# Optimization experiments

Measured on AMD Instinct MI355X. Metric: run time of the kernel, lower is better.

## Reference

```python
import jax, jax.numpy as jnp
import numpy as np

EPS = 1e-8  # matches PairwiseCosine eps clamp


def setup_inputs() -> dict:
    key = jax.random.key(0)
    k1, k2, k3 = jax.random.split(key, 3)
    B, N, M, D = 8, 2048, 2048, 256
    desc_src = jax.random.normal(k1, (B, N, D), dtype=jnp.float32)
    desc_dst = jax.random.normal(k2, (B, M, D), dtype=jnp.float32)
    points_dst = jax.random.uniform(k3, (B, M, 2), dtype=jnp.float32)
    return {"desc_src": desc_src, "desc_dst": desc_dst, "points_dst": points_dst}


def reference(desc_src, desc_dst, points_dst):
    # Pairwise cosine similarity: [B, N, M]
    xx = jnp.linalg.norm(desc_src, axis=-1, keepdims=True)          # [B, N, 1]
    yy = jnp.linalg.norm(desc_dst, axis=-1, keepdims=True)          # [B, M, 1]
    xy = jnp.einsum('bnd,bmd->bnm', desc_src, desc_dst)             # [B, N, M]
    sim = xy / jnp.maximum(xx * jnp.swapaxes(yy, 1, 2), EPS)
    # Best match per source descriptor
    confidence = jnp.max(sim, axis=2)                               # [B, N]
    idx = jnp.argmax(sim, axis=2)                                   # [B, N]
    # Gather matched destination points: [B, N, 2]
    matched = jnp.take_along_axis(points_dst, idx[:, :, None], axis=1)
    return (matched, confidence)
```

## Files before the change

kernel.cpp:

```cpp
#include <hip/hip_runtime.h>
#include <stdint.h>

constexpr int Bq = 8, Nq = 2048, Mq = 2048, Dq = 256;
constexpr int TILE = 128;
constexpr int KC = 32;
constexpr int NCH = Dq / KC;
constexpr int LDS_S = 40;

typedef float f32x4 __attribute__((ext_vector_type(4)));
typedef _Float16 f16x8 __attribute__((ext_vector_type(8)));
typedef _Float16 f16x4 __attribute__((ext_vector_type(4)));
typedef __fp16 fp16x2 __attribute__((ext_vector_type(2)));

__device__ __forceinline__ uint32_t f2sortable(float f) {
  uint32_t u = __float_as_uint(f);
  return (u & 0x80000000u) ? ~u : (u | 0x80000000u);
}
__device__ __forceinline__ float sortable2f(uint32_t s) {
  uint32_t u = (s & 0x80000000u) ? (s ^ 0x80000000u) : ~s;
  return __uint_as_float(u);
}

__device__ __forceinline__ void load16(float* d, const float* __restrict__ p) {
  *(float4*)&d[0]  = *(const float4*)(p + 0);
  *(float4*)&d[4]  = *(const float4*)(p + 4);
  *(float4*)&d[8]  = *(const float4*)(p + 8);
  *(float4*)&d[12] = *(const float4*)(p + 12);
}

__device__ __forceinline__ void split8(const float* x, f16x8* hi, f16x8* lo,
                                       float& sq) {
  union { f16x8 v; fp16x2 p[4]; } H, L;
#pragma unroll
  for (int j = 0; j < 4; ++j) {
    float x0 = x[2 * j], x1 = x[2 * j + 1];
    sq = fmaf(x0, x0, sq);
    sq = fmaf(x1, x1, sq);
    float h0 = __uint_as_float(__float_as_uint(x0) & 0xFFFFE000u);
    float h1 = __uint_as_float(__float_as_uint(x1) & 0xFFFFE000u);
    H.p[j] = __builtin_amdgcn_cvt_pkrtz(h0, h1);
    L.p[j] = __builtin_amdgcn_cvt_pkrtz(x0 - h0, x1 - h1);
  }
  *hi = H.v;
  *lo = L.v;
}


__global__ __launch_bounds__(256)
void prep_kernel(const float* __restrict__ src, const float* __restrict__ dst,
                 _Float16* __restrict__ Ah, _Float16* __restrict__ Al,
                 _Float16* __restrict__ Bh, _Float16* __restrict__ Bl,
                 float* __restrict__ invnx, float* __restrict__ invny) {
  const int lane = threadIdx.x & 63;
  const int wv = threadIdx.x >> 6;
  const int r = blockIdx.x * 4 + wv;

  const float* x;
  _Float16 *h, *l;
  float* inv;
  if (blockIdx.y == 0) { x = src; h = Ah; l = Al; inv = invnx; }
  else                 { x = dst; h = Bh; l = Bl; inv = invny; }

  float4 v = *(const float4*)(x + (size_t)r * Dq + lane * 4);
  float sq = 0.f;
  union { f16x4 v; fp16x2 p[2]; } H, L;
  float e[4] = {v.x, v.y, v.z, v.w};
#pragma unroll
  for (int j = 0; j < 2; ++j) {
    float x0 = e[2 * j], x1 = e[2 * j + 1];
    sq = fmaf(x0, x0, sq);
    sq = fmaf(x1, x1, sq);
    float h0 = __uint_as_float(__float_as_uint(x0) & 0xFFFFE000u);
    float h1 = __uint_as_float(__float_as_uint(x1) & 0xFFFFE000u);
    H.p[j] = __builtin_amdgcn_cvt_pkrtz(h0, h1);
    L.p[j] = __builtin_amdgcn_cvt_pkrtz(x0 - h0, x1 - h1);
  }
#pragma unroll
  for (int m = 1; m <= 32; m <<= 1) sq += __shfl_xor(sq, m);

  const int b = r >> 11, row = r & 2047;
  const int c = lane >> 3, ko = (lane & 7) * 4;
  size_t idx = ((size_t)(b * NCH + c) * 2048 + row) * KC + ko;
  *(f16x4*)&h[idx] = H.v;
  *(f16x4*)&l[idx] = L.v;
  if (lane == 0) inv[r] = 1.0f / sqrtf(sq);
}

__device__ __forceinline__ void stage(const _Float16* g, _Float16* l, int lane) {
  const char* gc = (const char*)g + lane * 16;
  char* lc = (char*)l;
#pragma unroll
  for (int i = 0; i < 8; ++i)
    __builtin_amdgcn_global_load_lds(
        (const __attribute__((address_space(1))) void*)(gc + i * 1024),
        (__attribute__((address_space(3))) void*)(lc + i * 1024),
        16, 0, 0);
}


__global__ __launch_bounds__(256, 2)
void simmax_mfma(const _Float16* __restrict__ Ah, const _Float16* __restrict__ Al,
                 const _Float16* __restrict__ Bh, const _Float16* __restrict__ Bl,
                 const float* __restrict__ invnx, const float* __restrict__ invny,
                 unsigned long long* __restrict__ best) {
  __shared__ __align__(16) _Float16 lds[2][4][TILE][KC];

  const int orig = blockIdx.x;
  const int logical = (orig & 7) * 256 + (orig >> 3);
  const int b = logical >> 8;
  const int nt = (logical >> 4) & 15;
  const int mt = logical & 15;

  const int tid = threadIdx.x;
  const int lane = tid & 63;
  const int wave = tid >> 6;
  const int wy = wave >> 1, wx = wave & 1;
  const int ln15 = lane & 15, lq = lane >> 4;

  const _Float16* garr = (wave == 0) ? Ah : (wave == 1) ? Al
                        : (wave == 2) ? Bh : Bl;
  const int grow = ((wave < 2) ? nt : mt) * TILE;
  const _Float16* g0 = garr + ((size_t)(b * NCH) * 2048 + grow) * KC;
  constexpr size_t CSTR = (size_t)2048 * KC;

  f32x4 acc[4][4];
#pragma unroll
  for (int i = 0; i < 4; ++i)
#pragma unroll
    for (int j = 0; j < 4; ++j) acc[i][j] = (f32x4){0.f, 0.f, 0.f, 0.f};

  stage(g0, &lds[0][wave][0][0], lane);
  __syncthreads();

#pragma unroll
  for (int c = 0; c < NCH; ++c) {
    const int cb = c & 1;
    if (c + 1 < NCH)
      stage(g0 + (size_t)(c + 1) * CSTR, &lds[cb ^ 1][wave][0][0], lane);

    f16x8 bhf[4], blf[4];
#pragma unroll
    for (int ct = 0; ct < 4; ++ct) {
      const int rb = wx * 64 + ct * 16 + ln15;
      bhf[ct] = *(const f16x8*)&lds[cb][2][rb][lq * 8];
      blf[ct] = *(const f16x8*)&lds[cb][3][rb][lq * 8];
    }
#pragma unroll
    for (int rt = 0; rt < 4; ++rt) {
      const int ra = wy * 64 + rt * 16 + ln15;
      f16x8 ahf = *(const f16x8*)&lds[cb][0][ra][lq * 8];
      f16x8 alf = *(const f16x8*)&lds[cb][1][ra][lq * 8];
#pragma unroll
      for (int ct = 0; ct < 4; ++ct) {
        acc[rt][ct] = __builtin_amdgcn_mfma_f32_16x16x32_f16(ahf, bhf[ct], acc[rt][ct], 0, 0, 0);
        acc[rt][ct] = __builtin_amdgcn_mfma_f32_16x16x32_f16(ahf, blf[ct], acc[rt][ct], 0, 0, 0);
        acc[rt][ct] = __builtin_amdgcn_mfma_f32_16x16x32_f16(alf, bhf[ct], acc[rt][ct], 0, 0, 0);
      }
    }
    if (c + 1 < NCH) __syncthreads();
  }

  float invy[4];
#pragma unroll
  for (int ct = 0; ct < 4; ++ct)
    invy[ct] = invny[(size_t)b * Mq + mt * TILE + wx * 64 + ct * 16 + ln15];

#pragma unroll
  for (int rt = 0; rt < 4; ++rt) {
#pragma unroll
    for (int reg = 0; reg < 4; ++reg) {
      float bq = -1e30f;
      int bc = 0x7FFFFFFF;
#pragma unroll
      for (int ct = 0; ct < 4; ++ct) {
        float q = acc[rt][ct][reg] * invy[ct];
        int cg = mt * TILE + wx * 64 + ct * 16 + ln15;
        if (q > bq || (q == bq && cg < bc)) { bq = q; bc = cg; }
      }
#pragma unroll
      for (int m = 1; m <= 8; m <<= 1) {
        float q2 = __shfl_xor(bq, m);
        int c2 = __shfl_xor(bc, m);
        if (q2 > bq || (q2 == bq && c2 < bc)) { bq = q2; bc = c2; }
      }
      if (ln15 == 0) {
        int rloc = wy * 64 + rt * 16 + lq * 4 + reg;
        float conf = bq * invnx[(size_t)b * Nq + nt * TILE + rloc];
        unsigned long long p =
            ((unsigned long long)(f2sortable(conf) ^ 0x80000000u) << 32) |
            (uint32_t)(~(uint32_t)bc);
        atomicMax((long long*)&best[(size_t)b * Nq + nt * TILE + rloc],
                  (long long)p);
      }
    }
  }
}

__global__ __launch_bounds__(256, 3)
void simmax_kernel(const float* __restrict__ src, const float* __restrict__ dst,
                   unsigned long long* __restrict__ best) {
  __shared__ _Float16 Ah[TILE][LDS_S], Al[TILE][LDS_S];
  __shared__ _Float16 Bh[TILE][LDS_S], Bl[TILE][LDS_S];
  __shared__ float invnx_s[TILE], invny_s[TILE];

  const int b = blockIdx.z, nt = blockIdx.y, mt = blockIdx.x;
  const int tid = threadIdx.x;
  const int lane = tid & 63;
  const int wave = tid >> 6;
  const int wy = wave >> 1, wx = wave & 1;
  const int ln15 = lane & 15, lq = lane >> 4;

  const int sr = tid >> 1;
  const int sk = (tid & 1) * 16;
  const float* Ag = src + ((size_t)(b * Nq + nt * TILE + sr)) * Dq + sk;
  const float* Bg = dst + ((size_t)(b * Mq + mt * TILE + sr)) * Dq + sk;

  f32x4 acc[4][4];
#pragma unroll
  for (int i = 0; i < 4; ++i)
#pragma unroll
    for (int j = 0; j < 4; ++j) acc[i][j] = (f32x4){0.f, 0.f, 0.f, 0.f};
  float sqa = 0.f, sqb = 0.f;

  float av[16], bv[16];
  load16(av, Ag);
  load16(bv, Bg);

  for (int c = 0; c < NCH; ++c) {
    f16x8 ah2[2], al2[2], bh2[2], bl2[2];
    split8(&av[0], &ah2[0], &al2[0], sqa);
    split8(&av[8], &ah2[1], &al2[1], sqa);
    split8(&bv[0], &bh2[0], &bl2[0], sqb);
    split8(&bv[8], &bh2[1], &bl2[1], sqb);
    __syncthreads();
    *(f16x8*)&Ah[sr][sk]     = ah2[0];
    *(f16x8*)&Ah[sr][sk + 8] = ah2[1];
    *(f16x8*)&Al[sr][sk]     = al2[0];
    *(f16x8*)&Al[sr][sk + 8] = al2[1];
    *(f16x8*)&Bh[sr][sk]     = bh2[0];
    *(f16x8*)&Bh[sr][sk + 8] = bh2[1];
    *(f16x8*)&Bl[sr][sk]     = bl2[0];
    *(f16x8*)&Bl[sr][sk + 8] = bl2[1];
    __syncthreads();

    if (c + 1 < NCH) {
      load16(av, Ag + (c + 1) * KC);
      load16(bv, Bg + (c + 1) * KC);
    }

    f16x8 bhf[4], blf[4];
#pragma unroll
    for (int ct = 0; ct < 4; ++ct) {
      int rowb = wx * 64 + ct * 16 + ln15;
      bhf[ct] = *(const f16x8*)&Bh[rowb][lq * 8];
      blf[ct] = *(const f16x8*)&Bl[rowb][lq * 8];
    }
#pragma unroll
    for (int rt = 0; rt < 4; ++rt) {
      int rowa = wy * 64 + rt * 16 + ln15;
      f16x8 ahf = *(const f16x8*)&Ah[rowa][lq * 8];
      f16x8 alf = *(const f16x8*)&Al[rowa][lq * 8];
#pragma unroll
      for (int ct = 0; ct < 4; ++ct) {
        acc[rt][ct] = __builtin_amdgcn_mfma_f32_16x16x32_f16(ahf, bhf[ct], acc[rt][ct], 0, 0, 0);
        acc[rt][ct] = __builtin_amdgcn_mfma_f32_16x16x32_f16(ahf, blf[ct], acc[rt][ct], 0, 0, 0);
        acc[rt][ct] = __builtin_amdgcn_mfma_f32_16x16x32_f16(alf, bhf[ct], acc[rt][ct], 0, 0, 0);
      }
    }
  }

  sqa += __shfl_xor(sqa, 1);
  sqb += __shfl_xor(sqb, 1);
  if ((tid & 1) == 0) {
    invnx_s[sr] = 1.0f / sqrtf(sqa);
    invny_s[sr] = 1.0f / sqrtf(sqb);
  }
  __syncthreads();

  float invny[4];
#pragma unroll
  for (int ct = 0; ct < 4; ++ct) invny[ct] = invny_s[wx * 64 + ct * 16 + ln15];

#pragma unroll
  for (int rt = 0; rt < 4; ++rt) {
#pragma unroll
    for (int reg = 0; reg < 4; ++reg) {
      float bq = -1e30f;
      int bc = 0x7FFFFFFF;
#pragma unroll
      for (int ct = 0; ct < 4; ++ct) {
        float q = acc[rt][ct][reg] * invny[ct];
        int cg = mt * TILE + wx * 64 + ct * 16 + ln15;
        if (q > bq || (q == bq && cg < bc)) { bq = q; bc = cg; }
      }
#pragma unroll
      for (int m = 1; m <= 8; m <<= 1) {
        float q2 = __shfl_xor(bq, m);
        int c2 = __shfl_xor(bc, m);
        if (q2 > bq || (q2 == bq && c2 < bc)) { bq = q2; bc = c2; }
      }
      if (ln15 == 0) {
        int rloc = wy * 64 + rt * 16 + lq * 4 + reg;
        float conf = bq * invnx_s[rloc];
        unsigned long long p =
            ((unsigned long long)(f2sortable(conf) ^ 0x80000000u) << 32) |
            (uint32_t)(~(uint32_t)bc);
        atomicMax((long long*)&best[(size_t)b * Nq + nt * TILE + rloc],
                  (long long)p);
      }
    }
  }
}

__global__ void finalize_kernel(const unsigned long long* __restrict__ best,
                                const float* __restrict__ pts,
                                float* __restrict__ out) {
  int i = blockIdx.x * blockDim.x + threadIdx.x;
  if (i >= Bq * Nq) return;
  unsigned long long p = best[i];
  uint32_t s = (uint32_t)(p >> 32) ^ 0x80000000u;
  int idx = (int)(~(uint32_t)(p & 0xFFFFFFFFull));
  float conf = sortable2f(s);
  int b = i / Nq;
  const float* q = pts + ((size_t)b * Mq + (size_t)idx) * 2;
  out[(size_t)i * 2 + 0] = q[0];
  out[(size_t)i * 2 + 1] = q[1];
  out[(size_t)(Bq * Nq) * 2 + i] = conf;
}

extern "C" void kernel_launch(void* const* d_in, const int* in_sizes, int n_in,
                              void* d_out, int out_size, void* d_ws, size_t ws_size,
                              hipStream_t stream) {
  const float* src = (const float*)d_in[0];
  const float* dst = (const float*)d_in[1];
  const float* pts = (const float*)d_in[2];
  float* out = (float*)d_out;

  unsigned long long* best = (unsigned long long*)d_ws;

  constexpr size_t BEST_B = (size_t)Bq * Nq * 8;
  constexpr size_t HL_B   = (size_t)Bq * 2048 * Dq * 2;
  constexpr size_t INV_B  = (size_t)Bq * 2048 * 4;
  constexpr size_t NEED   = BEST_B + 4 * HL_B + 2 * INV_B;

  if (ws_size >= NEED) {
    uint8_t* w = (uint8_t*)d_ws + BEST_B;
    _Float16* Ah = (_Float16*)(w);
    _Float16* Al = (_Float16*)(w + 1 * HL_B);
    _Float16* Bh = (_Float16*)(w + 2 * HL_B);
    _Float16* Bl = (_Float16*)(w + 3 * HL_B);
    float* invnx = (float*)(w + 4 * HL_B);
    float* invny = (float*)(w + 4 * HL_B + INV_B);

    prep_kernel<<<dim3(4096, 2, 1), 256, 0, stream>>>(src, dst, Ah, Al, Bh, Bl,
                                                      invnx, invny);
    simmax_mfma<<<dim3(2048, 1, 1), 256, 0, stream>>>(Ah, Al, Bh, Bl,
                                                      invnx, invny, best);
  } else {
    simmax_kernel<<<dim3(Mq / TILE, Nq / TILE, Bq), 256, 0, stream>>>(src, dst,
                                                                      best);
  }
  {
    int blocks = (Bq * Nq + 255) / 256;
    finalize_kernel<<<blocks, 256, 0, stream>>>(best, pts, out);
  }
}
```

Before: 164.2 us.

## Load A fragments directly from global, stage only B tiles in LDS

The A-operand (src hi/lo) fragments are now read straight from global memory into registers each chunk, and only the B tiles are staged through LDS. This halves the LDS footprint, so launch bounds go up to 4 blocks per CU and the chunk loop is only partially unrolled. The aim is less LDS traffic and higher occupancy. In exchange, A loads become uncoalesced-ish direct global reads with exposed latency that is not double-buffered, and A data is shared less across waves in the block.

Result: slower. 170.5 us (+3.8%).

```diff
diff --git a/kernel.cpp b/kernel.cpp
--- a/kernel.cpp
+++ b/kernel.cpp
@@ -86,24 +86,26 @@
   if (lane == 0) inv[r] = 1.0f / sqrtf(sq);
 }
 
-__device__ __forceinline__ void stage(const _Float16* g, _Float16* l, int lane) {
+
+constexpr size_t CSTR = (size_t)2048 * KC;
+
+__device__ __forceinline__ void stageB(const _Float16* g, _Float16* l, int lane) {
   const char* gc = (const char*)g + lane * 16;
   char* lc = (char*)l;
 #pragma unroll
-  for (int i = 0; i < 8; ++i)
+  for (int i = 0; i < 4; ++i)
     __builtin_amdgcn_global_load_lds(
         (const __attribute__((address_space(1))) void*)(gc + i * 1024),
         (__attribute__((address_space(3))) void*)(lc + i * 1024),
         16, 0, 0);
 }
 
-
-__global__ __launch_bounds__(256, 2)
+__global__ __launch_bounds__(256, 4)
 void simmax_mfma(const _Float16* __restrict__ Ah, const _Float16* __restrict__ Al,
                  const _Float16* __restrict__ Bh, const _Float16* __restrict__ Bl,
                  const float* __restrict__ invnx, const float* __restrict__ invny,
                  unsigned long long* __restrict__ best) {
-  __shared__ __align__(16) _Float16 lds[2][4][TILE][KC];
+  __shared__ __align__(16) _Float16 lds[2][2][TILE][KC];
 
   const int orig = blockIdx.x;
   const int logical = (orig & 7) * 256 + (orig >> 3);
@@ -117,11 +119,15 @@
   const int wy = wave >> 1, wx = wave & 1;
   const int ln15 = lane & 15, lq = lane >> 4;
 
-  const _Float16* garr = (wave == 0) ? Ah : (wave == 1) ? Al
-                        : (wave == 2) ? Bh : Bl;
-  const int grow = ((wave < 2) ? nt : mt) * TILE;
-  const _Float16* g0 = garr + ((size_t)(b * NCH) * 2048 + grow) * KC;
-  constexpr size_t CSTR = (size_t)2048 * KC;
+  const _Float16* gB0 = ((wave >> 1) == 0 ? Bh : Bl) +
+      ((size_t)(b * NCH) * 2048 + mt * TILE) * KC + (wave & 1) * 2048;
+  _Float16* ldsW0 = &lds[0][wave >> 1][0][0] + (wave & 1) * 2048;
+  _Float16* ldsW1 = &lds[1][wave >> 1][0][0] + (wave & 1) * 2048;
+
+  const size_t rbA =
+      ((size_t)(b * NCH) * 2048 + nt * TILE + wy * 64 + ln15) * KC + lq * 8;
+  const _Float16* pAh = Ah + rbA;
+  const _Float16* pAl = Al + rbA;
 
   f32x4 acc[4][4];
 #pragma unroll
@@ -129,32 +135,38 @@
 #pragma unroll
     for (int j = 0; j < 4; ++j) acc[i][j] = (f32x4){0.f, 0.f, 0.f, 0.f};
 
-  stage(g0, &lds[0][wave][0][0], lane);
+  stageB(gB0, ldsW0, lane);
   __syncthreads();
 
-#pragma unroll
+#pragma unroll 2
   for (int c = 0; c < NCH; ++c) {
     const int cb = c & 1;
     if (c + 1 < NCH)
-      stage(g0 + (size_t)(c + 1) * CSTR, &lds[cb ^ 1][wave][0][0], lane);
+      stageB(gB0 + (size_t)(c + 1) * CSTR, (cb ? ldsW0 : ldsW1), lane);
+
+    f16x8 ahf[4], alf[4];
+#pragma unroll
+    for (int rt = 0; rt < 4; ++rt) {
+      const size_t o = (size_t)c * CSTR + (size_t)rt * 16 * KC;
+      ahf[rt] = *(const f16x8*)(pAh + o);
+      alf[rt] = *(const f16x8*)(pAl + o);
+    }
 
     f16x8 bhf[4], blf[4];
 #pragma unroll
     for (int ct = 0; ct < 4; ++ct) {
       const int rb = wx * 64 + ct * 16 + ln15;
-      bhf[ct] = *(const f16x8*)&lds[cb][2][rb][lq * 8];
-      blf[ct] = *(const f16x8*)&lds[cb][3][rb][lq * 8];
-    }
+      bhf[ct] = *(const f16x8*)&lds[cb][0][rb][lq * 8];
+      blf[ct] = *(const f16x8*)&lds[cb][1][rb][lq * 8];
+    }
+
 #pragma unroll
     for (int rt = 0; rt < 4; ++rt) {
-      const int ra = wy * 64 + rt * 16 + ln15;
-      f16x8 ahf = *(const f16x8*)&lds[cb][0][ra][lq * 8];
-      f16x8 alf = *(const f16x8*)&lds[cb][1][ra][lq * 8];
 #pragma unroll
       for (int ct = 0; ct < 4; ++ct) {
-        acc[rt][ct] = __builtin_amdgcn_mfma_f32_16x16x32_f16(ahf, bhf[ct], acc[rt][ct], 0, 0, 0);
-        acc[rt][ct] = __builtin_amdgcn_mfma_f32_16x16x32_f16(ahf, blf[ct], acc[rt][ct], 0, 0, 0);
-        acc[rt][ct] = __builtin_amdgcn_mfma_f32_16x16x32_f16(alf, bhf[ct], acc[rt][ct], 0, 0, 0);
+        acc[rt][ct] = __builtin_amdgcn_mfma_f32_16x16x32_f16(ahf[rt], bhf[ct], acc[rt][ct], 0, 0, 0);
+        acc[rt][ct] = __builtin_amdgcn_mfma_f32_16x16x32_f16(ahf[rt], blf[ct], acc[rt][ct], 0, 0, 0);
+        acc[rt][ct] = __builtin_amdgcn_mfma_f32_16x16x32_f16(alf[rt], bhf[ct], acc[rt][ct], 0, 0, 0);
       }
     }
     if (c + 1 < NCH) __syncthreads();
```

## Replace simmax MFMA kernel with 256x256-tile, 8-wave, ring-buffered pipelined kernel

Applied to the files above, without the earlier changes.

Replaces the 128x128-tile, 4-wave MFMA kernel with a 256x256-tile, 512-thread kernel. It treats the three hi/lo split products as 12 K-steps streamed through an 8-slot LDS ring using direct global-to-LDS loads, with XOR-swizzled LDS columns, explicit vmcnt/lgkmcnt waits, barriers and setprio around MFMA bursts. Larger tiles raise operand reuse, and the phased prefetch is meant to overlap loads with matrix math. The cost is more accumulator registers (8x4 tiles per wave), a hand-tuned synchronisation schedule that depends on exact wait counts, and only 512 blocks in the grid.

After: 170.3 us. 1.04x slower.

```diff
diff --git a/kernel.cpp b/kernel.cpp
--- a/kernel.cpp
+++ b/kernel.cpp
@@ -6,6 +6,7 @@
 constexpr int KC = 32;
 constexpr int NCH = Dq / KC;
 constexpr int LDS_S = 40;
+constexpr int NKT = 12;
 
 typedef float f32x4 __attribute__((ext_vector_type(4)));
 typedef _Float16 f16x8 __attribute__((ext_vector_type(8)));
@@ -86,87 +87,117 @@
   if (lane == 0) inv[r] = 1.0f / sqrtf(sq);
 }
 
-__device__ __forceinline__ void stage(const _Float16* g, _Float16* l, int lane) {
-  const char* gc = (const char*)g + lane * 16;
-  char* lc = (char*)l;
+
+__global__ __launch_bounds__(512, 2)
+void simmax_8p(const _Float16* __restrict__ Ah, const _Float16* __restrict__ Al,
+               const _Float16* __restrict__ Bh, const _Float16* __restrict__ Bl,
+               const float* __restrict__ invnx, const float* __restrict__ invny,
+               unsigned long long* __restrict__ best) {
+  __shared__ __align__(16) _Float16 ring[8][256][KC];
+
+  const int orig = blockIdx.x;
+  const int logical = (orig & 7) * 64 + (orig >> 3);
+  const int b = logical >> 6;
+  const int nt = (logical >> 3) & 7;
+  const int mt = logical & 7;
+
+  const int tid = threadIdx.x, lane = tid & 63, w = tid >> 6;
+  const int wr = w >> 2, wc = w & 3;
+  const int ln15 = lane & 15, lq = lane >> 4;
+  const int qcol = (lq ^ ((ln15 >> 1) & 3)) * 8;
+
+  const size_t bBase = (size_t)b * (NCH * 2048 * KC);
+  const size_t aRow = (size_t)(nt * 256) * KC;
+  const size_t bRow = (size_t)(mt * 256) * KC;
+
+  const int U0 = w * 128 + lane;
+  const int r0 = U0 >> 2, q0 = U0 & 3;
+  const int so0 = r0 * KC + ((q0 ^ ((r0 >> 1) & 3)) << 3);
+
+  char* const ldsB = (char*)&ring[0][0][0];
+
+  f32x4 acc[8][4];
 #pragma unroll
   for (int i = 0; i < 8; ++i)
+#pragma unroll
+    for (int j = 0; j < 4; ++j) acc[i][j] = (f32x4){0.f, 0.f, 0.f, 0.f};
+  f16x8 bf[4];
+
+#pragma unroll
+  for (int u = 0; u < 4; ++u) {
+    const _Float16* arr = (u & 1) ? Bh : Ah;
+    const _Float16* src = arr + bBase + (size_t)(u >> 1) * 65536 +
+                          ((u & 1) ? bRow : aRow) + so0;
+    char* dst = ldsB + (size_t)u * 16384 + w * 2048;
     __builtin_amdgcn_global_load_lds(
-        (const __attribute__((address_space(1))) void*)(gc + i * 1024),
-        (__attribute__((address_space(3))) void*)(lc + i * 1024),
-        16, 0, 0);
-}
-
-
-__global__ __launch_bounds__(256, 2)
-void simmax_mfma(const _Float16* __restrict__ Ah, const _Float16* __restrict__ Al,
-                 const _Float16* __restrict__ Bh, const _Float16* __restrict__ Bl,
-                 const float* __restrict__ invnx, const float* __restrict__ invny,
-                 unsigned long long* __restrict__ best) {
-  __shared__ __align__(16) _Float16 lds[2][4][TILE][KC];
-
-  const int orig = blockIdx.x;
-  const int logical = (orig & 7) * 256 + (orig >> 3);
-  const int b = logical >> 8;
-  const int nt = (logical >> 4) & 15;
-  const int mt = logical & 15;
-
-  const int tid = threadIdx.x;
-  const int lane = tid & 63;
-  const int wave = tid >> 6;
-  const int wy = wave >> 1, wx = wave & 1;
-  const int ln15 = lane & 15, lq = lane >> 4;
-
-  const _Float16* garr = (wave == 0) ? Ah : (wave == 1) ? Al
-                        : (wave == 2) ? Bh : Bl;
-  const int grow = ((wave < 2) ? nt : mt) * TILE;
-  const _Float16* g0 = garr + ((size_t)(b * NCH) * 2048 + grow) * KC;
-  constexpr size_t CSTR = (size_t)2048 * KC;
-
-  f32x4 acc[4][4];
-#pragma unroll
-  for (int i = 0; i < 4; ++i)
-#pragma unroll
-    for (int j = 0; j < 4; ++j) acc[i][j] = (f32x4){0.f, 0.f, 0.f, 0.f};
-
-  stage(g0, &lds[0][wave][0][0], lane);
-  __syncthreads();
-
-#pragma unroll
-  for (int c = 0; c < NCH; ++c) {
-    const int cb = c & 1;
-    if (c + 1 < NCH)
-      stage(g0 + (size_t)(c + 1) * CSTR, &lds[cb ^ 1][wave][0][0], lane);
-
-    f16x8 bhf[4], blf[4];
-#pragma unroll
-    for (int ct = 0; ct < 4; ++ct) {
-      const int rb = wx * 64 + ct * 16 + ln15;
-      bhf[ct] = *(const f16x8*)&lds[cb][2][rb][lq * 8];
-      blf[ct] = *(const f16x8*)&lds[cb][3][rb][lq * 8];
-    }
-#pragma unroll
-    for (int rt = 0; rt < 4; ++rt) {
-      const int ra = wy * 64 + rt * 16 + ln15;
-      f16x8 ahf = *(const f16x8*)&lds[cb][0][ra][lq * 8];
-      f16x8 alf = *(const f16x8*)&lds[cb][1][ra][lq * 8];
-#pragma unroll
-      for (int ct = 0; ct < 4; ++ct) {
-        acc[rt][ct] = __builtin_amdgcn_mfma_f32_16x16x32_f16(ahf, bhf[ct], acc[rt][ct], 0, 0, 0);
-        acc[rt][ct] = __builtin_amdgcn_mfma_f32_16x16x32_f16(ahf, blf[ct], acc[rt][ct], 0, 0, 0);
-        acc[rt][ct] = __builtin_amdgcn_mfma_f32_16x16x32_f16(alf, bhf[ct], acc[rt][ct], 0, 0, 0);
-      }
-    }
-    if (c + 1 < NCH) __syncthreads();
-  }
+        (const __attribute__((address_space(1))) void*)src,
+        (__attribute__((address_space(3))) void*)dst, 16, 0, 0);
+    __builtin_amdgcn_global_load_lds(
+        (const __attribute__((address_space(1))) void*)(src + 512),
+        (__attribute__((address_space(3))) void*)(dst + 1024), 16, 0, 0);
+  }
+  asm volatile("s_waitcnt vmcnt(4)" ::: "memory");
+  __builtin_amdgcn_s_barrier();
+
+#define PHASE(Q, RG, KT)                                                        \
+  do {                                                                          \
+    constexpr int ks_ = (Q) >> 1, rt0_ = ((Q) & 1) * 4;                         \
+    f16x8 af_[4];                                                               \
+    _Pragma("unroll") for (int j = 0; j < 4; ++j)                               \
+      af_[j] = *(const f16x8*)&ring[(RG) * 4 + ks_ * 2]                         \
+          [wr * 128 + (rt0_ + j) * 16 + ln15][qcol];                            \
+    if ((Q & 1) == 0) {                                                         \
+      _Pragma("unroll") for (int ct = 0; ct < 4; ++ct)                          \
+        bf[ct] = *(const f16x8*)&ring[(RG) * 4 + ks_ * 2 + 1]                   \
+            [wc * 64 + ct * 16 + ln15][qcol];                                   \
+    }                                                                           \
+    {                                                                           \
+      int kte_ = ((KT) < NKT) ? (KT) : 0; \
+      int tau_ = kte_ >> 2;                                                     \
+      int c_ = 2 * (kte_ & 3) + ks_;                                            \
+      const _Float16* arr_;                                                     \
+      if ((Q) & 1) arr_ = (tau_ == 1) ? Bl : Bh;                                \
+      else         arr_ = (tau_ == 2) ? Al : Ah;                                \
+      const _Float16* src_ = arr_ + bBase + (size_t)c_ * 65536 +                \
+                             (((Q) & 1) ? bRow : aRow) + so0;                   \
+      char* dst_ = ldsB + (size_t)(((RG) ^ 1) * 4 + (Q)) * 16384 + w * 2048;    \
+      __builtin_amdgcn_global_load_lds(                                         \
+          (const __attribute__((address_space(1))) void*)src_,                  \
+          (__attribute__((address_space(3))) void*)dst_, 16, 0, 0);             \
+      __builtin_amdgcn_global_load_lds(                                         \
+          (const __attribute__((address_space(1))) void*)(src_ + 512),          \
+          (__attribute__((address_space(3))) void*)(dst_ + 1024), 16, 0, 0);    \
+    }                                                                           \
+    __builtin_amdgcn_s_barrier();                                               \
+    asm volatile("s_waitcnt lgkmcnt(0)" ::: "memory");                          \
+    __builtin_amdgcn_sched_barrier(0);                                          \
+    __builtin_amdgcn_s_setprio(1);                                              \
+    _Pragma("unroll") for (int j = 0; j < 4; ++j)                               \
+      _Pragma("unroll") for (int ct = 0; ct < 4; ++ct)                          \
+        acc[rt0_ + j][ct] = __builtin_amdgcn_mfma_f32_16x16x32_f16(             \
+            af_[j], bf[ct], acc[rt0_ + j][ct], 0, 0, 0);                        \
+    __builtin_amdgcn_s_setprio(0);                                              \
+    if ((Q) & 1) asm volatile("s_waitcnt vmcnt(4)" ::: "memory");               \
+    __builtin_amdgcn_s_barrier();                                               \
+  } while (0)
+
+#pragma unroll 1
+  for (int tt = 0; tt < NKT; tt += 2) {
+    PHASE(0, 0, tt + 1); PHASE(1, 0, tt + 1);
+    PHASE(2, 0, tt + 1); PHASE(3, 0, tt + 1);
+    PHASE(0, 1, tt + 2); PHASE(1, 1, tt + 2);
+    PHASE(2, 1, tt + 2); PHASE(3, 1, tt + 2);
+  }
+#undef PHASE
 
   float invy[4];
 #pragma unroll
   for (int ct = 0; ct < 4; ++ct)
-    invy[ct] = invny[(size_t)b * Mq + mt * TILE + wx * 64 + ct * 16 + ln15];
-
-#pragma unroll
-  for (int rt = 0; rt < 4; ++rt) {
+    invy[ct] = invny[(size_t)b * Mq + mt * 256 + wc * 64 + ct * 16 + ln15];
+  const float* invxp = invnx + (size_t)b * Nq + nt * 256;
+
+#pragma unroll
+  for (int rt = 0; rt < 8; ++rt) {
 #pragma unroll
     for (int reg = 0; reg < 4; ++reg) {
       float bq = -1e30f;
@@ -174,7 +205,7 @@
 #pragma unroll
       for (int ct = 0; ct < 4; ++ct) {
         float q = acc[rt][ct][reg] * invy[ct];
-        int cg = mt * TILE + wx * 64 + ct * 16 + ln15;
+        int cg = mt * 256 + wc * 64 + ct * 16 + ln15;
         if (q > bq || (q == bq && cg < bc)) { bq = q; bc = cg; }
       }
 #pragma unroll
@@ -184,12 +215,12 @@
         if (q2 > bq || (q2 == bq && c2 < bc)) { bq = q2; bc = c2; }
       }
       if (ln15 == 0) {
-        int rloc = wy * 64 + rt * 16 + lq * 4 + reg;
-        float conf = bq * invnx[(size_t)b * Nq + nt * TILE + rloc];
+        int rloc = wr * 128 + rt * 16 + lq * 4 + reg;
+        float conf = bq * invxp[rloc];
         unsigned long long p =
             ((unsigned long long)(f2sortable(conf) ^ 0x80000000u) << 32) |
             (uint32_t)(~(uint32_t)bc);
-        atomicMax((long long*)&best[(size_t)b * Nq + nt * TILE + rloc],
+        atomicMax((long long*)&best[(size_t)b * Nq + nt * 256 + rloc],
                   (long long)p);
       }
     }
@@ -199,8 +230,8 @@
 __global__ __launch_bounds__(256, 3)
 void simmax_kernel(const float* __restrict__ src, const float* __restrict__ dst,
                    unsigned long long* __restrict__ best) {
-  __shared__ _Float16 Ah[TILE][LDS_S], Al[TILE][LDS_S];
-  __shared__ _Float16 Bh[TILE][LDS_S], Bl[TILE][LDS_S];
+  __shared__ _Float16 Ahs[TILE][LDS_S], Als[TILE][LDS_S];
+  __shared__ _Float16 Bhs[TILE][LDS_S], Bls[TILE][LDS_S];
   __shared__ float invnx_s[TILE], invny_s[TILE];
 
   const int b = blockIdx.z, nt = blockIdx.y, mt = blockIdx.x;
@@ -233,14 +264,14 @@
     split8(&bv[0], &bh2[0], &bl2[0], sqb);
     split8(&bv[8], &bh2[1], &bl2[1], sqb);
     __syncthreads();
-    *(f16x8*)&Ah[sr][sk]     = ah2[0];
-    *(f16x8*)&Ah[sr][sk + 8] = ah2[1];
-    *(f16x8*)&Al[sr][sk]     = al2[0];
-    *(f16x8*)&Al[sr][sk + 8] = al2[1];
-    *(f16x8*)&Bh[sr][sk]     = bh2[0];
-    *(f16x8*)&Bh[sr][sk + 8] = bh2[1];
-    *(f16x8*)&Bl[sr][sk]     = bl2[0];
-    *(f16x8*)&Bl[sr][sk + 8] = bl2[1];
+    *(f16x8*)&Ahs[sr][sk]     = ah2[0];
+    *(f16x8*)&Ahs[sr][sk + 8] = ah2[1];
+    *(f16x8*)&Als[sr][sk]     = al2[0];
+    *(f16x8*)&Als[sr][sk + 8] = al2[1];
+    *(f16x8*)&Bhs[sr][sk]     = bh2[0];
+    *(f16x8*)&Bhs[sr][sk + 8] = bh2[1];
+    *(f16x8*)&Bls[sr][sk]     = bl2[0];
+    *(f16x8*)&Bls[sr][sk + 8] = bl2[1];
     __syncthreads();
 
     if (c + 1 < NCH) {
@@ -252,14 +283,14 @@
 #pragma unroll
     for (int ct = 0; ct < 4; ++ct) {
       int rowb = wx * 64 + ct * 16 + ln15;
-      bhf[ct] = *(const f16x8*)&Bh[rowb][lq * 8];
-      blf[ct] = *(const f16x8*)&Bl[rowb][lq * 8];
+      bhf[ct] = *(const f16x8*)&Bhs[rowb][lq * 8];
+      blf[ct] = *(const f16x8*)&Bls[rowb][lq * 8];
     }
 #pragma unroll
     for (int rt = 0; rt < 4; ++rt) {
       int rowa = wy * 64 + rt * 16 + ln15;
-      f16x8 ahf = *(const f16x8*)&Ah[rowa][lq * 8];
-      f16x8 alf = *(const f16x8*)&Al[rowa][lq * 8];
+      f16x8 ahf = *(const f16x8*)&Ahs[rowa][lq * 8];
+      f16x8 alf = *(const f16x8*)&Als[rowa][lq * 8];
 #pragma unroll
       for (int ct = 0; ct < 4; ++ct) {
         acc[rt][ct] = __builtin_amdgcn_mfma_f32_16x16x32_f16(ahf, bhf[ct], acc[rt][ct], 0, 0, 0);
@@ -277,9 +308,9 @@
   }
   __syncthreads();
 
-  float invny[4];
-#pragma unroll
-  for (int ct = 0; ct < 4; ++ct) invny[ct] = invny_s[wx * 64 + ct * 16 + ln15];
+  float invny_r[4];
+#pragma unroll
+  for (int ct = 0; ct < 4; ++ct) invny_r[ct] = invny_s[wx * 64 + ct * 16 + ln15];
 
 #pragma unroll
   for (int rt = 0; rt < 4; ++rt) {
@@ -289,7 +320,7 @@
       int bc = 0x7FFFFFFF;
 #pragma unroll
       for (int ct = 0; ct < 4; ++ct) {
-        float q = acc[rt][ct][reg] * invny[ct];
+        float q = acc[rt][ct][reg] * invny_r[ct];
         int cg = mt * TILE + wx * 64 + ct * 16 + ln15;
         if (q > bq || (q == bq && cg < bc)) { bq = q; bc = cg; }
       }
@@ -354,8 +385,8 @@
 
     prep_kernel<<<dim3(4096, 2, 1), 256, 0, stream>>>(src, dst, Ah, Al, Bh, Bl,
                                                       invnx, invny);
-    simmax_mfma<<<dim3(2048, 1, 1), 256, 0, stream>>>(Ah, Al, Bh, Bl,
-                                                      invnx, invny, best);
+    simmax_8p<<<dim3(512, 1, 1), 512, 0, stream>>>(Ah, Al, Bh, Bl,
+                                                   invnx, invny, best);
   } else {
     simmax_kernel<<<dim3(Mq / TILE, Nq / TILE, Bq), 256, 0, stream>>>(src, dst,
                                                                       best);
```
